# Optimization experiments

Hardware: AMD Instinct MI355X
Metric: run time of the kernel (lower is better)

The kernel has to match this reference:

```python
import jax, jax.numpy as jnp
import numpy as np

N_KERNELS = 11
B, Q, D, E, C = 128, 32, 512, 300, 128

def _kernel_mus(n):
    mus = [1.0]
    bs = 2.0 / (n - 1)
    mus.append(1 - bs / 2)
    for i in range(1, n - 1):
        mus.append(mus[i] - bs)
    return np.array(mus, dtype=np.float32)

def _kernel_sigmas(n):
    bs = 2.0 / (n - 1)
    return np.array([0.001] + [0.5 * bs] * (n - 1), dtype=np.float32)

def setup_inputs():
    key = jax.random.key(0)
    ks = jax.random.split(key, 10)
    return {
        "query_embeddings": jax.random.normal(ks[0], (B, Q, E), jnp.float32),
        "document_embeddings": jax.random.normal(ks[1], (B, D, E), jnp.float32),
        "query_pad_oov_mask": jnp.ones((B, Q), jnp.float32),
        "document_pad_oov_mask": jnp.ones((B, D), jnp.float32),
        "conv1_w": jax.random.normal(ks[2], (C, E, 1), jnp.float32) * 0.05,
        "conv1_b": jnp.zeros((C,), jnp.float32),
        "conv2_w": jax.random.normal(ks[3], (C, E, 2), jnp.float32) * 0.05,
        "conv2_b": jnp.zeros((C,), jnp.float32),
        "conv3_w": jax.random.normal(ks[4], (C, E, 3), jnp.float32) * 0.05,
        "conv3_b": jnp.zeros((C,), jnp.float32),
        "nn_scaler": jnp.full((1,), 0.01, jnp.float32),
        "dense_w": jax.random.uniform(ks[5], (1, N_KERNELS * 9), jnp.float32, -0.014, 0.014),
        "dense_b": jnp.zeros((1,), jnp.float32),
        "dense_mean_w": jax.random.normal(ks[6], (1, N_KERNELS * 9), jnp.float32) * 0.05,
        "dense_mean_b": jnp.zeros((1,), jnp.float32),
        "dense_comb_w": jax.random.normal(ks[7], (1, 2), jnp.float32) * 0.5,
    }

def _conv_relu(x, w, b):
    # x: [B, L, E] -> [B, L, C]; right-pad by k-1 (ConstantPad1d((0, k-1))) so out len == L
    k = w.shape[-1]
    y = jax.lax.conv_general_dilated(x.transpose(0, 2, 1), w, (1,), [(0, k - 1)],
                                     dimension_numbers=("NCH", "OIH", "NCH"))
    return jax.nn.relu(y + b[None, :, None]).transpose(0, 2, 1)

def _kernel_pool(q, d, qd_mask, q_mask, doc_len, mu, sigma, scaler):
    # cosine matrix (AllenNLP CosineMatrixAttention: L2-normalize with 1e-13 tie-break)
    qn = q / (jnp.linalg.norm(q, axis=-1, keepdims=True) + 1e-13)
    dn = d / (jnp.linalg.norm(d, axis=-1, keepdims=True) + 1e-13)
    cos = jnp.einsum("bqc,bdc->bqd", qn, dn) * qd_mask
    # RBF soft-histogram kernels over the similarity matrix: [B,q,d,K]
    kr = jnp.exp(-(cos[..., None] - mu) ** 2 / (2.0 * sigma ** 2)) * qd_mask[..., None]
    pkq = kr.sum(axis=2)  # [B, Q, K]
    std = (jnp.log(jnp.clip(pkq, 1e-10)) * scaler * q_mask[..., None]).sum(axis=1)
    pkq_mean = pkq / doc_len[:, None, None]
    mean = (jnp.log(jnp.clip(pkq_mean, 1e-10)) * scaler * q_mask[..., None]).sum(axis=1)
    return std, mean

def _forward(qe, de, qm, dm, c1w, c1b, c2w, c2b, c3w, c3b, ns, dw, db, dmw, dmb, dcw):
    mu = jnp.asarray(_kernel_mus(N_KERNELS))
    sigma = jnp.asarray(_kernel_sigmas(N_KERNELS))
    qd_mask = qm[:, :, None] * dm[:, None, :]
    doc_len = dm.sum(axis=1)
    convs = [(c1w, c1b), (c2w, c2b), (c3w, c3b)]
    q_res = [_conv_relu(qe, w, b) for w, b in convs]
    d_res = [_conv_relu(de, w, b) for w, b in convs]
    std_list, mean_list = [], []
    for qr in q_res:
        for dr in d_res:
            s, m = _kernel_pool(qr, dr, qd_mask, qm, doc_len, mu, sigma, ns)
            std_list.append(s)
            mean_list.append(m)
    all_grams = jnp.concatenate(std_list, axis=1)       # [B, 9*K]
    all_grams_mean = jnp.concatenate(mean_list, axis=1)
    dense_out = all_grams @ dw.T + db
    dense_mean_out = all_grams_mean @ dmw.T + dmb
    comb = jnp.concatenate([dense_out, dense_mean_out], axis=1) @ dcw.T
    return comb[:, 0]

def reference(query_embeddings, document_embeddings, query_pad_oov_mask, document_pad_oov_mask,
              conv1_w, conv1_b, conv2_w, conv2_b, conv3_w, conv3_b,
              nn_scaler, dense_w, dense_b, dense_mean_w, dense_mean_b, dense_comb_w):
    return _forward(query_embeddings, document_embeddings, query_pad_oov_mask, document_pad_oov_mask,
                    conv1_w, conv1_b, conv2_w, conv2_b, conv3_w, conv3_b,
                    nn_scaler, dense_w, dense_b, dense_mean_w, dense_mean_b, dense_comb_w)
```

## Files before the change

kernel.cpp:

```cpp
#include <hip/hip_runtime.h>
#include <hip/hip_bf16.h>
#include <cstdint>

namespace {

typedef __bf16 bf8v __attribute__((ext_vector_type(8)));
typedef __bf16 bf4v __attribute__((ext_vector_type(4)));
typedef float  f4v  __attribute__((ext_vector_type(4)));
typedef uint32_t u32x4 __attribute__((ext_vector_type(4)));

constexpr int kB = 128;
constexpr int kQ = 32;
constexpr int kD = 512;
constexpr int kE = 300;
constexpr int kC = 128;
constexpr int kK = 11;

constexpr size_t QNB_B = 491520;
constexpr size_t DNB_B = 3637248;
constexpr size_t PKQ_B = 53968896;

constexpr float LOG2E = 1.4426950408889634f;

constexpr int XS_STRIDE = 336;
constexpr int TB_STRIDE = 136;

__global__ __launch_bounds__(256) void prep_kernel(
    const float* __restrict__ w1, const float* __restrict__ w2, const float* __restrict__ w3,
    __bf16* __restrict__ wb)
{
  int i = blockIdx.x * 256 + threadIdx.x;
  if (i >= 245760) return;
  int el = i & 31;
  int sc = i >> 5;
  int c  = sc & 127;
  int chunk = sc >> 7;
  int slab = chunk / 10;
  int ks = chunk - slab * 10;
  int e = ks * 32 + el;
  float v = 0.f;
  if (e < kE) {
    if (slab == 0)      v = w1[c * kE + e];
    else if (slab <= 2) v = w2[(c * kE + e) * 2 + (slab - 1)];
    else                v = w3[(c * kE + e) * 3 + (slab - 3)];
  }
  wb[i] = (__bf16)v;
}

template<int VM>
__device__ __forceinline__ void wait_vm() {
  if constexpr (VM == 2) asm volatile("s_waitcnt vmcnt(2)" ::: "memory");
  else                   asm volatile("s_waitcnt vmcnt(0)" ::: "memory");
  __builtin_amdgcn_sched_barrier(0);
}

__device__ __forceinline__ void issue2(u32x4 (&Wset)[2], const __bf16* p) {
  asm volatile("global_load_dwordx4 %0, %1, off"             : "=v"(Wset[0]) : "v"(p) : "memory");
  asm volatile("global_load_dwordx4 %0, %1, off offset:1024" : "=v"(Wset[1]) : "v"(p) : "memory");
}

__device__ __forceinline__ void mfma4(bf8v A0, bf8v A1, u32x4 (&Ws)[2], f4v (&acc)[2][2]) {
  #pragma unroll
  for (int nf = 0; nf < 2; ++nf) {
    bf8v Wf = __builtin_bit_cast(bf8v, Ws[nf]);
    acc[0][nf] = __builtin_amdgcn_mfma_f32_16x16x32_bf16(A0, Wf, acc[0][nf], 0, 0, 0);
    acc[1][nf] = __builtin_amdgcn_mfma_f32_16x16x32_bf16(A1, Wf, acc[1][nf], 0, 0, 0);
  }
}

template<int NJ, int CH0>
__device__ __forceinline__ void conv_grp(
    const __bf16* __restrict__ wb, const __bf16* __restrict__ Xs,
    int w, int lr, int g, f4v (&acc)[2][2])
{
  const __bf16* wl = wb + (size_t)CH0 * 4096 + (w * 32 + lr) * 32 + g * 8;
  const int ae = g * 8;

  u32x4 W0[2], W1[2];
  issue2(W0, wl);
  issue2(W1, wl + 4096);
  const __bf16* wnext = wl + 2 * 4096;

  #pragma unroll
  for (int j = 0; j < NJ; ++j) {
    const __bf16* xr = Xs + (size_t)(lr + j) * XS_STRIDE + ae;
    const int nks = (j == NJ - 1) ? 8 : 10;
    #pragma unroll 1
    for (int ks = 0; ks < nks; ks += 2) {
      bf8v A0 = *(const bf8v*)(xr + ks * 32);
      bf8v A1 = *(const bf8v*)(xr + 16 * XS_STRIDE + ks * 32);
      wait_vm<2>();
      mfma4(A0, A1, W0, acc);
      issue2(W0, wnext); wnext += 4096;
      bf8v B0 = *(const bf8v*)(xr + ks * 32 + 32);
      bf8v B1 = *(const bf8v*)(xr + 16 * XS_STRIDE + ks * 32 + 32);
      wait_vm<2>();
      mfma4(B0, B1, W1, acc);
      issue2(W1, wnext); wnext += 4096;
    }
  }
  const __bf16* xr = Xs + (size_t)(lr + NJ - 1) * XS_STRIDE + ae;
  bf8v A0 = *(const bf8v*)(xr + 8 * 32);
  bf8v A1 = *(const bf8v*)(xr + 16 * XS_STRIDE + 8 * 32);
  wait_vm<2>();
  mfma4(A0, A1, W0, acc);
  bf8v B0 = *(const bf8v*)(xr + 9 * 32);
  bf8v B1 = *(const bf8v*)(xr + 16 * XS_STRIDE + 9 * 32);
  wait_vm<0>();
  mfma4(B0, B1, W1, acc);
}

__global__ __launch_bounds__(256, 5) void conv_fused(
    const float* __restrict__ qe, const float* __restrict__ de,
    const __bf16* __restrict__ wb,
    const float* __restrict__ b1, const float* __restrict__ b2, const float* __restrict__ b3,
    __bf16* __restrict__ qnb, __bf16* __restrict__ dnb)
{
  const int bx = blockIdx.x;
  const int b  = blockIdx.y;
  const bool isq = (bx == 0);
  const int L  = isq ? kQ : kD;
  const int p0 = isq ? 0 : (bx - 1) * 32;
  const float* xsrc = (isq ? qe : de) + (size_t)b * L * kE;

  const int t = threadIdx.x;
  const int w = t >> 6, l = t & 63;
  const int lr = l & 15, g = l >> 4;

  __shared__ __align__(16) __bf16 Xs[34 * XS_STRIDE];
  __shared__ __align__(16) __bf16 tbuf[32 * TB_STRIDE];
  __shared__ float sqs4[4][32];

  for (int idx = t; idx < 34 * 82; idx += 256) {
    int row = idx / 82, c4 = idx - row * 82;
    int gp = p0 + row;
    float4 v = make_float4(0.f, 0.f, 0.f, 0.f);
    if (gp < L && c4 < 75) v = *(const float4*)(xsrc + (size_t)gp * kE + c4 * 4);
    bf4v hv = { (__bf16)v.x, (__bf16)v.y, (__bf16)v.z, (__bf16)v.w };
    *(bf4v*)&Xs[row * XS_STRIDE + c4 * 4] = hv;
  }
  __syncthreads();

  #pragma unroll
  for (int grp = 0; grp < 3; ++grp) {
    f4v acc[2][2];
    #pragma unroll
    for (int mf = 0; mf < 2; ++mf)
      #pragma unroll
      for (int nf = 0; nf < 2; ++nf)
        acc[mf][nf] = (f4v)0.f;

    if (grp == 0)      conv_grp<1, 0>(wb, Xs, w, lr, g, acc);
    else if (grp == 1) conv_grp<2, 10>(wb, Xs, w, lr, g, acc);
    else               conv_grp<3, 30>(wb, Xs, w, lr, g, acc);

    const float* bias = (grp == 0) ? b1 : ((grp == 1) ? b2 : b3);
    float bvs[2];
    #pragma unroll
    for (int nf = 0; nf < 2; ++nf) bvs[nf] = bias[w * 32 + nf * 16 + lr];

    f4v ssum[2];
    #pragma unroll
    for (int mf = 0; mf < 2; ++mf) {
      ssum[mf] = (f4v)0.f;
      #pragma unroll
      for (int nf = 0; nf < 2; ++nf)
        #pragma unroll
        for (int r = 0; r < 4; ++r) {
          float y = fmaxf(acc[mf][nf][r] + bvs[nf], 0.f);
          acc[mf][nf][r] = y;
          ssum[mf][r] += y * y;
        }
    }
    #pragma unroll
    for (int off = 1; off < 16; off <<= 1)
      #pragma unroll
      for (int mf = 0; mf < 2; ++mf)
        #pragma unroll
        for (int r = 0; r < 4; ++r)
          ssum[mf][r] += __shfl_xor(ssum[mf][r], off);

    if (lr == 0) {
      #pragma unroll
      for (int mf = 0; mf < 2; ++mf)
        *(float4*)&sqs4[w][mf * 16 + g * 4] = *(float4*)&ssum[mf];
    }
    __syncthreads();
    float inv[2][4];
    #pragma unroll
    for (int mf = 0; mf < 2; ++mf)
      #pragma unroll
      for (int r = 0; r < 4; ++r) {
        int row = mf * 16 + g * 4 + r;
        float s = sqs4[0][row] + sqs4[1][row] + sqs4[2][row] + sqs4[3][row];
        inv[mf][r] = 1.f / (sqrtf(s) + 1e-13f);
      }
    #pragma unroll
    for (int mf = 0; mf < 2; ++mf)
      #pragma unroll
      for (int nf = 0; nf < 2; ++nf)
        #pragma unroll
        for (int r = 0; r < 4; ++r) {
          int row = mf * 16 + g * 4 + r;
          int c = w * 32 + nf * 16 + lr;
          tbuf[row * TB_STRIDE + c] = (__bf16)(acc[mf][nf][r] * inv[mf][r]);
        }
    __syncthreads();
    __bf16* outp = (isq ? qnb : dnb) + ((size_t)(grp * kB + b)) * L * kC + (size_t)p0 * kC;
    #pragma unroll
    for (int ci = t; ci < 512; ci += 256) {
      bf8v v = *(const bf8v*)&tbuf[(ci >> 4) * TB_STRIDE + (ci & 15) * 8];
      *(bf8v*)(outp + ci * 8) = v;
    }
    asm volatile("s_waitcnt vmcnt(0)" ::: "memory");
    __syncthreads();
  }
}

__global__ __launch_bounds__(256) void pool_mfma(
    const __bf16* __restrict__ qnb,
    const __bf16* __restrict__ dnb,
    const float* __restrict__ qmask,
    const float* __restrict__ dmask,
    float* __restrict__ pkq)
{
  const int pair = blockIdx.x;
  const int b = blockIdx.y;
  const int qi = pair / 3, dj = pair - qi * 3;
  const __bf16* qb = qnb + ((size_t)qi * kB + b) * kQ * kC;
  const __bf16* db = dnb + ((size_t)dj * kB + b) * kD * kC;

  const int t = threadIdx.x;
  const int w = t >> 6, l = t & 63;
  const int lr = l & 15, g = l >> 4;

  __shared__ float red[4][2][16][kK];

  bf8v Bq[2][4];
  #pragma unroll
  for (int qt = 0; qt < 2; ++qt)
    #pragma unroll
    for (int kc = 0; kc < 4; ++kc)
      Bq[qt][kc] = *(const bf8v*)&qb[(size_t)(qt * 16 + lr) * kC + kc * 32 + g * 8];

  float qmv[2];
  #pragma unroll
  for (int qt = 0; qt < 2; ++qt) qmv[qt] = qmask[b * kQ + qt * 16 + lr];

  const float c1[10] = { 129.84255368f, 100.98865286f,  72.13475204f,  43.28085123f,  14.42695041f,
                         -14.42695041f, -43.28085123f, -72.13475204f, -100.98865286f, -129.84255368f };
  const float c2[10] = { -58.42914915f, -35.34602850f, -18.03368801f, -6.49212768f, -0.72134752f,
                          -0.72134752f,  -6.49212768f, -18.03368801f, -35.34602850f, -58.42914915f };
  const float C50 = -50.f * LOG2E;
  const float C0  = -500000.f * LOG2E;

  float pk[2][kK];
  #pragma unroll
  for (int qt = 0; qt < 2; ++qt)
    #pragma unroll
    for (int k = 0; k < kK; ++k) pk[qt][k] = 0.f;

  const int dt0 = w * 8;
  bf8v An[4];
  #pragma unroll
  for (int kc = 0; kc < 4; ++kc)
    An[kc] = *(const bf8v*)&db[(size_t)(dt0 * 16 + lr) * kC + kc * 32 + g * 8];

  for (int dtl = 0; dtl < 8; ++dtl) {
    const int drow0 = (dt0 + dtl) * 16;
    bf8v Ac[4];
    #pragma unroll
    for (int kc = 0; kc < 4; ++kc) Ac[kc] = An[kc];
    if (dtl < 7) {
      #pragma unroll
      for (int kc = 0; kc < 4; ++kc)
        An[kc] = *(const bf8v*)&db[(size_t)(drow0 + 16 + lr) * kC + kc * 32 + g * 8];
    }
    f4v acc0 = (f4v)0.f, acc1 = (f4v)0.f;
    #pragma unroll
    for (int kc = 0; kc < 4; ++kc) {
      acc0 = __builtin_amdgcn_mfma_f32_16x16x32_bf16(Ac[kc], Bq[0][kc], acc0, 0, 0, 0);
      acc1 = __builtin_amdgcn_mfma_f32_16x16x32_bf16(Ac[kc], Bq[1][kc], acc1, 0, 0, 0);
    }
    float4 dmv = *(const float4*)&dmask[b * kD + drow0 + g * 4];
    #pragma unroll
    for (int qt = 0; qt < 2; ++qt) {
      const f4v& a = qt ? acc1 : acc0;
      #pragma unroll
      for (int r = 0; r < 4; ++r) {
        float dm = (r == 0) ? dmv.x : (r == 1) ? dmv.y : (r == 2) ? dmv.z : dmv.w;
        float off = fmaf(dm, 1000.f, -1000.f);
        float s = a[r] * qmv[qt] * dm;
        float s2 = s * s;
        float base = fmaf(s2, C50, off);
        float dd = s - 1.f;
        pk[qt][0] += exp2f(fmaf(dd * dd, C0, off));
        #pragma unroll
        for (int k = 0; k < 10; ++k)
          pk[qt][k + 1] += exp2f(fmaf(c1[k], s, base) + c2[k]);
      }
    }
  }

  #pragma unroll
  for (int off = 16; off < 64; off <<= 1)
    #pragma unroll
    for (int qt = 0; qt < 2; ++qt)
      #pragma unroll
      for (int k = 0; k < kK; ++k)
        pk[qt][k] += __shfl_xor(pk[qt][k], off);

  if (l < 16) {
    #pragma unroll
    for (int qt = 0; qt < 2; ++qt)
      #pragma unroll
      for (int k = 0; k < kK; ++k)
        red[w][qt][lr][k] = pk[qt][k];
  }
  __syncthreads();
  for (int i = t; i < 2 * 16 * kK; i += 256) {
    int qt = i / (16 * kK);
    int rem = i - qt * 16 * kK;
    int lq = rem / kK, k = rem - lq * kK;
    float v = red[0][qt][lq][k] + red[1][qt][lq][k] + red[2][qt][lq][k] + red[3][qt][lq][k];
    int q = qt * 16 + lq;
    pkq[(((size_t)pair * kB + b) * kQ + q) * kK + k] = v * qmask[b * kQ + q];
  }
}

__global__ __launch_bounds__(128) void finalize_kernel(
    const float* __restrict__ pkq, const float* __restrict__ qmask,
    const float* __restrict__ dmask, const float* __restrict__ nsp,
    const float* __restrict__ dw, const float* __restrict__ dbp,
    const float* __restrict__ dmw, const float* __restrict__ dmbp,
    const float* __restrict__ dcw, float* __restrict__ out)
{
  const int b = blockIdx.x;
  const int t = threadIdx.x;
  __shared__ float sh[4];
  float dl = 0.f;
  for (int d = t; d < kD; d += 128) dl += dmask[b * kD + d];
  #pragma unroll
  for (int off = 1; off < 64; off <<= 1) dl += __shfl_xor(dl, off);
  if ((t & 63) == 0) sh[t >> 6] = dl;
  __syncthreads();
  const float idl = 1.f / (sh[0] + sh[1]);
  const float sc = nsp[0];
  float ps = 0.f, pm = 0.f;
  for (int i = t; i < 99; i += 128) {
    int pr = i / kK, kk = i - pr * kK;
    const float* base = pkq + ((size_t)pr * kB + b) * kQ * kK + kk;
    float ss = 0.f, sm = 0.f;
    for (int q = 0; q < kQ; ++q) {
      float v = base[q * kK];
      float qq = qmask[b * kQ + q];
      ss += __logf(fmaxf(v, 1e-10f)) * qq;
      sm += __logf(fmaxf(v * idl, 1e-10f)) * qq;
    }
    ps += dw[i] * ss;
    pm += dmw[i] * sm;
  }
  ps *= sc; pm *= sc;
  #pragma unroll
  for (int off = 1; off < 64; off <<= 1) { ps += __shfl_xor(ps, off); pm += __shfl_xor(pm, off); }
  __syncthreads();
  if ((t & 63) == 0) { sh[t >> 6] = ps; sh[2 + (t >> 6)] = pm; }
  __syncthreads();
  if (t == 0) {
    float PS = sh[0] + sh[1] + dbp[0];
    float PM = sh[2] + sh[3] + dmbp[0];
    out[b] = dcw[0] * PS + dcw[1] * PM;
  }
}

}

extern "C" void kernel_launch(void* const* d_in, const int* in_sizes, int n_in,
                              void* d_out, int out_size, void* d_ws, size_t ws_size,
                              hipStream_t stream) {
  const float* qe  = (const float*)d_in[0];
  const float* de  = (const float*)d_in[1];
  const float* qm  = (const float*)d_in[2];
  const float* dm  = (const float*)d_in[3];
  const float* w1  = (const float*)d_in[4];
  const float* b1  = (const float*)d_in[5];
  const float* w2  = (const float*)d_in[6];
  const float* b2  = (const float*)d_in[7];
  const float* w3  = (const float*)d_in[8];
  const float* b3  = (const float*)d_in[9];
  const float* ns  = (const float*)d_in[10];
  const float* dw  = (const float*)d_in[11];
  const float* db  = (const float*)d_in[12];
  const float* dmw = (const float*)d_in[13];
  const float* dmb = (const float*)d_in[14];
  const float* dcw = (const float*)d_in[15];
  float* out = (float*)d_out;

  char* wsb = (char*)d_ws;
  __bf16* wb  = (__bf16*)wsb;
  __bf16* qnb = (__bf16*)(wsb + QNB_B);
  __bf16* dnb = (__bf16*)(wsb + DNB_B);
  float*  pkq = (float*)(wsb + PKQ_B);

  prep_kernel<<<960, 256, 0, stream>>>(w1, w2, w3, wb);
  conv_fused<<<dim3(17, kB), 256, 0, stream>>>(qe, de, wb, b1, b2, b3, qnb, dnb);
  pool_mfma<<<dim3(9, kB), 256, 0, stream>>>(qnb, dnb, qm, dm, pkq);
  finalize_kernel<<<kB, 128, 0, stream>>>(pkq, qm, dm, ns, dw, db, dmw, dmb, dcw, out);
}
```

Before: 162.7 us.

## Deepen weight prefetch pipeline to five stages in conv MFMA loop

Replaces the two-buffer weight prefetch in the conv GEMM loop with a fully unrolled five-deep ring of global loads, using graded vmcnt waits. LDS activation fragments are software-pipelined one step ahead. The memory clobber is removed from the load asm, and launch bounds drop from 5 to 4 blocks per CU to make room for the extra registers. The aim is to hide global-load latency for the weights, at the cost of lower occupancy and larger code.

```diff
diff --git a/kernel.cpp b/kernel.cpp
--- a/kernel.cpp
+++ b/kernel.cpp
@@ -47,16 +47,18 @@
   wb[i] = (__bf16)v;
 }
 
-template<int VM>
-__device__ __forceinline__ void wait_vm() {
-  if constexpr (VM == 2) asm volatile("s_waitcnt vmcnt(2)" ::: "memory");
-  else                   asm volatile("s_waitcnt vmcnt(0)" ::: "memory");
+__device__ __forceinline__ void wait_vmc(int n) {
+  if (n >= 8)      asm volatile("s_waitcnt vmcnt(8)" ::: "memory");
+  else if (n == 6) asm volatile("s_waitcnt vmcnt(6)" ::: "memory");
+  else if (n == 4) asm volatile("s_waitcnt vmcnt(4)" ::: "memory");
+  else if (n == 2) asm volatile("s_waitcnt vmcnt(2)" ::: "memory");
+  else             asm volatile("s_waitcnt vmcnt(0)" ::: "memory");
   __builtin_amdgcn_sched_barrier(0);
 }
 
 __device__ __forceinline__ void issue2(u32x4 (&Wset)[2], const __bf16* p) {
-  asm volatile("global_load_dwordx4 %0, %1, off"             : "=v"(Wset[0]) : "v"(p) : "memory");
-  asm volatile("global_load_dwordx4 %0, %1, off offset:1024" : "=v"(Wset[1]) : "v"(p) : "memory");
+  asm volatile("global_load_dwordx4 %0, %1, off"             : "=v"(Wset[0]) : "v"(p));
+  asm volatile("global_load_dwordx4 %0, %1, off offset:1024" : "=v"(Wset[1]) : "v"(p));
 }
 
 __device__ __forceinline__ void mfma4(bf8v A0, bf8v A1, u32x4 (&Ws)[2], f4v (&acc)[2][2]) {
@@ -73,44 +75,35 @@
     const __bf16* __restrict__ wb, const __bf16* __restrict__ Xs,
     int w, int lr, int g, f4v (&acc)[2][2])
 {
+  constexpr int N = NJ * 10;
   const __bf16* wl = wb + (size_t)CH0 * 4096 + (w * 32 + lr) * 32 + g * 8;
-  const int ae = g * 8;
-
-  u32x4 W0[2], W1[2];
-  issue2(W0, wl);
-  issue2(W1, wl + 4096);
-  const __bf16* wnext = wl + 2 * 4096;
-
-  #pragma unroll
-  for (int j = 0; j < NJ; ++j) {
-    const __bf16* xr = Xs + (size_t)(lr + j) * XS_STRIDE + ae;
-    const int nks = (j == NJ - 1) ? 8 : 10;
-    #pragma unroll 1
-    for (int ks = 0; ks < nks; ks += 2) {
-      bf8v A0 = *(const bf8v*)(xr + ks * 32);
-      bf8v A1 = *(const bf8v*)(xr + 16 * XS_STRIDE + ks * 32);
-      wait_vm<2>();
-      mfma4(A0, A1, W0, acc);
-      issue2(W0, wnext); wnext += 4096;
-      bf8v B0 = *(const bf8v*)(xr + ks * 32 + 32);
-      bf8v B1 = *(const bf8v*)(xr + 16 * XS_STRIDE + ks * 32 + 32);
-      wait_vm<2>();
-      mfma4(B0, B1, W1, acc);
-      issue2(W1, wnext); wnext += 4096;
-    }
-  }
-  const __bf16* xr = Xs + (size_t)(lr + NJ - 1) * XS_STRIDE + ae;
-  bf8v A0 = *(const bf8v*)(xr + 8 * 32);
-  bf8v A1 = *(const bf8v*)(xr + 16 * XS_STRIDE + 8 * 32);
-  wait_vm<2>();
-  mfma4(A0, A1, W0, acc);
-  bf8v B0 = *(const bf8v*)(xr + 9 * 32);
-  bf8v B1 = *(const bf8v*)(xr + 16 * XS_STRIDE + 9 * 32);
-  wait_vm<0>();
-  mfma4(B0, B1, W1, acc);
-}
-
-__global__ __launch_bounds__(256, 5) void conv_fused(
+  const __bf16* xb0 = Xs + (size_t)lr * XS_STRIDE + g * 8;
+  const __bf16* xb1 = xb0 + 16 * XS_STRIDE;
+
+  u32x4 W[5][2];
+  #pragma unroll
+  for (int p = 0; p < 5 && p < N; ++p) issue2(W[p], wl + (size_t)p * 4096);
+
+  bf8v Ac0 = *(const bf8v*)xb0;
+  bf8v Ac1 = *(const bf8v*)xb1;
+
+  #pragma unroll
+  for (int s = 0; s < N; ++s) {
+    bf8v An0, An1;
+    if (s + 1 < N) {
+      const int j1 = (s + 1) / 10, k1 = (s + 1) - ((s + 1) / 10) * 10;
+      An0 = *(const bf8v*)(xb0 + j1 * XS_STRIDE + k1 * 32);
+      An1 = *(const bf8v*)(xb1 + j1 * XS_STRIDE + k1 * 32);
+    }
+    const int rem = N - s;
+    wait_vmc(rem >= 5 ? 8 : 2 * rem - 2);
+    mfma4(Ac0, Ac1, W[s % 5], acc);
+    if (s + 5 < N) issue2(W[s % 5], wl + (size_t)(s + 5) * 4096);
+    Ac0 = An0; Ac1 = An1;
+  }
+}
+
+__global__ __launch_bounds__(256, 4) void conv_fused(
     const float* __restrict__ qe, const float* __restrict__ de,
     const __bf16* __restrict__ wb,
     const float* __restrict__ b1, const float* __restrict__ b2, const float* __restrict__ b3,
```

New measurement: 167.7 us. 3.1% more time.
